# Optimization experiments

Hardware: AMD Instinct MI355X
Metric: run time of the kernel (lower is better)

Reference implementation:

```python
import jax, jax.numpy as jnp
import numpy as np

B, N, DIN, DINNER, DOUT, W = 4, 8192, 512, 512, 512, 128


def setup_inputs() -> dict:
    key = jax.random.key(0)
    k1, k2, k3 = jax.random.split(key, 3)
    x = jax.random.normal(k1, (B, N, DIN), jnp.float32)
    # torch Linear weights: (out_features, in_features)
    w_qkv = jax.random.normal(k2, (3 * DINNER, DIN), jnp.float32) * (DIN ** -0.5)
    w_out = jax.random.normal(k3, (DOUT, DINNER), jnp.float32) * (DINNER ** -0.5)
    b_out = jnp.zeros((DOUT,), jnp.float32)
    return {"x": x, "w_qkv": w_qkv, "w_out": w_out, "b_out": b_out}


def reference(x, w_qkv, w_out, b_out):
    b, n, _ = x.shape
    w = W
    scale = DINNER ** -0.5
    pad = (-n) % w  # pad_to_multiple along seq dim (static)
    xp = jnp.pad(x, ((0, 0), (0, pad), (0, 0)))
    qkv = jnp.einsum('bnd,ed->bne', xp, w_qkv)  # to_qkv, no bias
    q, k, v = jnp.split(qkv, 3, axis=-1)
    win = lambda t: t.reshape(b, -1, w, DINNER)  # b (w n) d -> b w n d
    q, k, v = win(q), win(k), win(v)
    # prepend one zero bucket to k, then overlap prev/current windows.
    kp = jnp.pad(k, ((0, 0), (1, 0), (0, 0), (0, 0)))
    k2 = jnp.concatenate((kp[:, :-1], kp[:, 1:]), axis=2)  # (b, nb, 2w, d)
    # NOTE: source bug replicated — v is also built from k, not v.
    v2 = jnp.concatenate((kp[:, :-1], kp[:, 1:]), axis=2)
    sim = jnp.einsum('bwid,bwjd->bwij', q, k2) * scale  # (b, nb, w, 2w)
    i, j = w, 2 * w
    mask = jnp.triu(jnp.ones((i, j), bool), j - i + 1)
    sim = jnp.where(mask, -jnp.finfo(sim.dtype).max, sim)
    attn = jax.nn.softmax(sim, axis=-1)
    out = jnp.einsum('bwij,bwjd->bwid', attn, v2)
    out = out.reshape(b, -1, DINNER)[:, :n]
    return jnp.einsum('bnd,od->bno', out, w_out) + b_out
```

## Files before the change

kernel.cpp:

```cpp
#include <hip/hip_runtime.h>
#include <cstdint>
#include <cstddef>

typedef float f32x4 __attribute__((ext_vector_type(4)));
typedef short s16x8 __attribute__((ext_vector_type(8)));
typedef short s16x4 __attribute__((ext_vector_type(4)));

#define MFMA_BF16(a, b, c) __builtin_amdgcn_mfma_f32_16x16x32_bf16((a), (b), (c), 0, 0, 0)

#define GLD16(g, l)                                                            \
  __builtin_amdgcn_global_load_lds(                                            \
      (const __attribute__((address_space(1))) void*)(g),                      \
      (__attribute__((address_space(3))) void*)(l), 16, 0, 0)

__device__ __forceinline__ unsigned short f2bf(float f) {
  unsigned int u = __float_as_uint(f);
  u += 0x7FFFu + ((u >> 16) & 1u);
  return (unsigned short)(u >> 16);
}

__device__ __forceinline__ s16x8 cvt8(const float* __restrict__ src) {
  const float4 f0 = *(const float4*)src;
  const float4 f1 = *(const float4*)(src + 4);
  s16x8 h;
  h[0] = (short)f2bf(f0.x); h[1] = (short)f2bf(f0.y);
  h[2] = (short)f2bf(f0.z); h[3] = (short)f2bf(f0.w);
  h[4] = (short)f2bf(f1.x); h[5] = (short)f2bf(f1.y);
  h[6] = (short)f2bf(f1.z); h[7] = (short)f2bf(f1.w);
  return h;
}

#define XN 16777216
#define WQN 524288
__global__ __launch_bounds__(256)
void cvt_bf16(const float* __restrict__ x, const float* __restrict__ wqkv,
              const float* __restrict__ wout, unsigned short* __restrict__ xb,
              unsigned short* __restrict__ wb, unsigned short* __restrict__ wob) {
  const size_t i = (size_t)(blockIdx.x * 256 + threadIdx.x) * 8;
  const float* src;
  unsigned short* dst;
  if (i < XN) { src = x + i; dst = xb + i; }
  else if (i < XN + WQN) { src = wqkv + (i - XN); dst = wb + (i - XN); }
  else { src = wout + (i - XN - WQN); dst = wob + (i - XN - WQN); }
  *(s16x8*)dst = cvt8(src);
}

__global__ __launch_bounds__(256)
void gemm_qk(const unsigned short* __restrict__ xb, const unsigned short* __restrict__ wb,
             unsigned short* __restrict__ Q, unsigned short* __restrict__ K) {
  __shared__ unsigned short As[128 * 64];
  __shared__ unsigned short Bs[128 * 64];
  const int t = threadIdx.x, lane = t & 63, wid = t >> 6;
  const int wm = wid >> 1, wn = wid & 1;
  const int nl = lane & 15, quad = lane >> 4;
  const int sub = lane >> 3, lblk = (lane & 7) ^ sub;
  const int l = blockIdx.x;
  const int xcd = l & 7, g = l >> 3;
  const int mt = (g >> 3) * 8 + xcd, nt = g & 7;
  const int m0 = mt * 128, n0 = nt * 128;

  const f32x4 zero = {0.f, 0.f, 0.f, 0.f};
  f32x4 acc[4][4];
#pragma unroll
  for (int i = 0; i < 4; ++i)
#pragma unroll
    for (int j = 0; j < 4; ++j) acc[i][j] = zero;

  const unsigned short* gX = xb + (size_t)(m0 + wid * 32 + sub) * 512 + lblk * 8;
  const unsigned short* gW = wb + (size_t)(n0 + wid * 32 + sub) * 512 + lblk * 8;

  for (int kc = 0; kc < 512; kc += 64) {
#pragma unroll
    for (int ii = 0; ii < 4; ++ii) {
      GLD16(gW + kc + (size_t)(ii * 8) * 512, &As[(wid * 32 + ii * 8) * 64]);
      GLD16(gX + kc + (size_t)(ii * 8) * 512, &Bs[(wid * 32 + ii * 8) * 64]);
    }
    __syncthreads();
#pragma unroll
    for (int ks = 0; ks < 2; ++ks) {
      s16x8 af[4], bf[4];
#pragma unroll
      for (int i = 0; i < 4; ++i)
        af[i] = *(const s16x8*)&As[(wm * 64 + i * 16 + nl) * 64 +
                                   (((ks * 4 + quad) ^ (nl & 7)) * 8)];
#pragma unroll
      for (int j = 0; j < 4; ++j)
        bf[j] = *(const s16x8*)&Bs[(wn * 64 + j * 16 + nl) * 64 +
                                   (((ks * 4 + quad) ^ (nl & 7)) * 8)];
#pragma unroll
      for (int i = 0; i < 4; ++i)
#pragma unroll
        for (int j = 0; j < 4; ++j) acc[i][j] = MFMA_BF16(af[i], bf[j], acc[i][j]);
    }
    __syncthreads();
  }
#pragma unroll
  for (int i = 0; i < 4; ++i) {
    const int n = n0 + wm * 64 + i * 16 + quad * 4;
    unsigned short* base = (n < 512 ? Q : K);
    const int nn = n & 511;
#pragma unroll
    for (int j = 0; j < 4; ++j) {
      const int m = m0 + wn * 64 + j * 16 + nl;
      s16x4 h;
#pragma unroll
      for (int r = 0; r < 4; ++r) h[r] = (short)f2bf(acc[i][j][r]);
      *(s16x4*)&base[(size_t)m * 512 + nn] = h;
    }
  }
}

__global__ __launch_bounds__(256)
void gemm_kwt(const unsigned short* __restrict__ K, const unsigned short* __restrict__ wob,
              unsigned short* __restrict__ KWT) {
  __shared__ unsigned short As[128 * 64];
  __shared__ unsigned short Bs[128 * 64];
  const int t = threadIdx.x, lane = t & 63, wid = t >> 6;
  const int wm = wid >> 1, wn = wid & 1;
  const int nl = lane & 15, quad = lane >> 4;
  const int sub = lane >> 3, lblk = (lane & 7) ^ sub;
  const int l = blockIdx.x;
  const int xcd = l & 7, g = l >> 3;
  const int mt = (g >> 2) * 8 + xcd, nt = g & 3;
  const int m0 = mt * 128, n0 = nt * 128;

  const f32x4 zero = {0.f, 0.f, 0.f, 0.f};
  f32x4 acc[4][4];
#pragma unroll
  for (int i = 0; i < 4; ++i)
#pragma unroll
    for (int j = 0; j < 4; ++j) acc[i][j] = zero;

  const unsigned short* gA = K + (size_t)(m0 + wid * 32 + sub) * 512 + lblk * 8;
  const unsigned short* gB = wob + (size_t)(n0 + wid * 32 + sub) * 512 + lblk * 8;

  for (int kc = 0; kc < 512; kc += 64) {
#pragma unroll
    for (int ii = 0; ii < 4; ++ii) {
      GLD16(gA + kc + (size_t)(ii * 8) * 512, &As[(wid * 32 + ii * 8) * 64]);
      GLD16(gB + kc + (size_t)(ii * 8) * 512, &Bs[(wid * 32 + ii * 8) * 64]);
    }
    __syncthreads();
#pragma unroll
    for (int ks = 0; ks < 2; ++ks) {
      s16x8 af[4], bf[4];
#pragma unroll
      for (int i = 0; i < 4; ++i)
        af[i] = *(const s16x8*)&As[(wm * 64 + i * 16 + nl) * 64 +
                                   (((ks * 4 + quad) ^ (nl & 7)) * 8)];
#pragma unroll
      for (int j = 0; j < 4; ++j)
        bf[j] = *(const s16x8*)&Bs[(wn * 64 + j * 16 + nl) * 64 +
                                   (((ks * 4 + quad) ^ (nl & 7)) * 8)];
#pragma unroll
      for (int i = 0; i < 4; ++i)
#pragma unroll
        for (int j = 0; j < 4; ++j) acc[i][j] = MFMA_BF16(af[i], bf[j], acc[i][j]);
    }
    __syncthreads();
  }
#pragma unroll
  for (int i = 0; i < 4; ++i) {
    const int ms = m0 + wm * 64 + i * 16 + quad * 4;
    const int b = ms >> 13, ns = ms & 8191;
#pragma unroll
    for (int j = 0; j < 4; ++j) {
      const int o = n0 + wn * 64 + j * 16 + nl;
      s16x4 h;
#pragma unroll
      for (int r = 0; r < 4; ++r) h[r] = (short)f2bf(acc[i][j][r]);
      *(s16x4*)&KWT[(size_t)(b * 512 + o) * 8192 + ns] = h;
    }
  }
}

__global__ __launch_bounds__(256)
void attn64(const unsigned short* __restrict__ Q, const unsigned short* __restrict__ K,
            const unsigned short* __restrict__ KWT, const float* __restrict__ bias,
            float* __restrict__ out) {
  __shared__ unsigned short Ps[64 * 256];
  __shared__ float redm[256];
  __shared__ float reds[256];
  const int t = threadIdx.x, lane = t & 63, wid = t >> 6;
  const int wn = wid;
  const int nl = lane & 15, quad = lane >> 4;
  const int bx = blockIdx.x;
  const int xcd = bx & 7, half = (bx >> 3) & 1, g = bx >> 4;
  const int wb = g * 8 + xcd, b = wb >> 6, w = wb & 63;

  const f32x4 zero = {0.f, 0.f, 0.f, 0.f};
  f32x4 acc[4][4];
#pragma unroll
  for (int i = 0; i < 4; ++i)
#pragma unroll
    for (int j = 0; j < 4; ++j) acc[i][j] = zero;

  const unsigned short* Qb = Q + (size_t)(b * 8192 + w * 128 + half * 64) * 512;
  const unsigned short* Kb = K + (size_t)(b * 8192) * 512;

  const unsigned short* qptr[4];
  const unsigned short* kptr[4];
#pragma unroll
  for (int i = 0; i < 4; ++i) qptr[i] = Qb + (size_t)(i * 16 + nl) * 512;
#pragma unroll
  for (int j = 0; j < 4; ++j) {
    int seq = w * 128 - 128 + wn * 64 + j * 16 + nl;
    if (seq < 0) seq = 0;
    kptr[j] = Kb + (size_t)seq * 512;
  }

#pragma unroll 2
  for (int kc = 0; kc < 512; kc += 64) {
#pragma unroll
    for (int ks = 0; ks < 2; ++ks) {
      const int off = kc + (ks * 4 + quad) * 8;
      s16x8 af[4], bf[4];
#pragma unroll
      for (int i = 0; i < 4; ++i) af[i] = *(const s16x8*)(qptr[i] + off);
#pragma unroll
      for (int j = 0; j < 4; ++j) bf[j] = *(const s16x8*)(kptr[j] + off);
      __builtin_amdgcn_s_setprio(1);
#pragma unroll
      for (int i = 0; i < 4; ++i)
#pragma unroll
        for (int j = 0; j < 4; ++j) acc[i][j] = MFMA_BF16(af[i], bf[j], acc[i][j]);
      __builtin_amdgcn_s_setprio(0);
    }
  }

  const float scale = 0.04419417382415922f;
  float rmax[4][4];
#pragma unroll
  for (int i = 0; i < 4; ++i) {
#pragma unroll
    for (int r = 0; r < 4; ++r) {
      const int qrow = half * 64 + i * 16 + quad * 4 + r;
      float mx = -3.4e38f;
#pragma unroll
      for (int j = 0; j < 4; ++j) {
        const int col = wn * 64 + j * 16 + nl;
        float v = acc[i][j][r] * scale;
        if (col >= 128 && col - 128 > qrow) v = -3.0e38f;
        if (w == 0 && col < 128) v = 0.0f;
        acc[i][j][r] = v;
        mx = fmaxf(mx, v);
      }
      rmax[i][r] = mx;
    }
  }
#pragma unroll
  for (int off = 1; off < 16; off <<= 1)
#pragma unroll
    for (int i = 0; i < 4; ++i)
#pragma unroll
      for (int r = 0; r < 4; ++r)
        rmax[i][r] = fmaxf(rmax[i][r], __shfl_xor(rmax[i][r], off, 64));
  if (nl == 0) {
#pragma unroll
    for (int i = 0; i < 4; ++i)
#pragma unroll
      for (int r = 0; r < 4; ++r)
        redm[(i * 16 + quad * 4 + r) * 4 + wn] = rmax[i][r];
  }
  __syncthreads();
  float rsum[4][4];
#pragma unroll
  for (int i = 0; i < 4; ++i) {
#pragma unroll
    for (int r = 0; r < 4; ++r) {
      const f32x4 mv = *(const f32x4*)&redm[(i * 16 + quad * 4 + r) * 4];
      const float m = fmaxf(fmaxf(mv[0], mv[1]), fmaxf(mv[2], mv[3]));
      float s = 0.f;
#pragma unroll
      for (int j = 0; j < 4; ++j) {
        const float p = __expf(acc[i][j][r] - m);
        acc[i][j][r] = p;
        s += p;
      }
      rsum[i][r] = s;
    }
  }
#pragma unroll
  for (int off = 1; off < 16; off <<= 1)
#pragma unroll
    for (int i = 0; i < 4; ++i)
#pragma unroll
      for (int r = 0; r < 4; ++r) rsum[i][r] += __shfl_xor(rsum[i][r], off, 64);
  if (nl == 0) {
#pragma unroll
    for (int i = 0; i < 4; ++i)
#pragma unroll
      for (int r = 0; r < 4; ++r)
        reds[(i * 16 + quad * 4 + r) * 4 + wn] = rsum[i][r];
  }
  __syncthreads();
#pragma unroll
  for (int i = 0; i < 4; ++i) {
#pragma unroll
    for (int r = 0; r < 4; ++r) {
      const int row = i * 16 + quad * 4 + r;
      const f32x4 sv = *(const f32x4*)&reds[row * 4];
      const float inv = 1.0f / (sv[0] + sv[1] + sv[2] + sv[3]);
#pragma unroll
      for (int j = 0; j < 4; ++j) {
        const int col = wn * 64 + j * 16 + nl;
        float pv = acc[i][j][r] * inv;
        if (w == 0 && col < 128) pv = 0.0f;
        const int cb = col >> 3;
        Ps[row * 256 + (((cb ^ (row & 7)) << 3) | (col & 7))] = f2bf(pv);
      }
    }
  }
  __syncthreads();

  const int seqbase = w * 128 - 128;
#pragma unroll 1
  for (int och = 0; och < 4; ++och) {
    f32x4 acc2[4][2];
#pragma unroll
    for (int i = 0; i < 4; ++i)
#pragma unroll
      for (int j = 0; j < 2; ++j) acc2[i][j] = zero;
    const unsigned short* bp0 =
        KWT + (size_t)(b * 512 + och * 128 + wn * 32 + nl) * 8192;
    const unsigned short* bp1 = bp0 + (size_t)16 * 8192;
#pragma unroll
    for (int kch = 0; kch < 4; ++kch) {
#pragma unroll
      for (int ks = 0; ks < 2; ++ks) {
        int sq = seqbase + kch * 64 + (ks * 4 + quad) * 8;
        if (sq < 0) sq = 0;
        const int kb = kch * 8 + ks * 4 + quad;
        s16x8 af[4], bf[2];
#pragma unroll
        for (int i = 0; i < 4; ++i)
          af[i] = *(const s16x8*)&Ps[(i * 16 + nl) * 256 + ((kb ^ (nl & 7)) << 3)];
        bf[0] = *(const s16x8*)(bp0 + sq);
        bf[1] = *(const s16x8*)(bp1 + sq);
        __builtin_amdgcn_s_setprio(1);
#pragma unroll
        for (int i = 0; i < 4; ++i) {
          acc2[i][0] = MFMA_BF16(af[i], bf[0], acc2[i][0]);
          acc2[i][1] = MFMA_BF16(af[i], bf[1], acc2[i][1]);
        }
        __builtin_amdgcn_s_setprio(0);
      }
    }
#pragma unroll
    for (int i = 0; i < 4; ++i) {
      const int seq = w * 128 + half * 64 + i * 16 + quad * 4;
      float* dst = out + (size_t)(b * 8192 + seq) * 512;
#pragma unroll
      for (int j = 0; j < 2; ++j) {
        const int o = och * 128 + wn * 32 + j * 16 + nl;
        const float bo = bias[o];
#pragma unroll
        for (int r = 0; r < 4; ++r) dst[(size_t)r * 512 + o] = acc2[i][j][r] + bo;
      }
    }
  }
}

extern "C" void kernel_launch(void* const* d_in, const int* in_sizes, int n_in,
                              void* d_out, int out_size, void* d_ws, size_t ws_size,
                              hipStream_t stream) {
  const float* x = (const float*)d_in[0];
  const float* w_qkv = (const float*)d_in[1];
  const float* w_out = (const float*)d_in[2];
  const float* b_out = (const float*)d_in[3];
  float* out = (float*)d_out;

  char* ws = (char*)d_ws;
  unsigned short* Q = (unsigned short*)ws;
  unsigned short* K = (unsigned short*)(ws + (size_t)33554432);
  unsigned short* xb = (unsigned short*)(ws + (size_t)67108864);
  unsigned short* KWT = (unsigned short*)(ws + (size_t)67108864);
  unsigned short* wb = (unsigned short*)(ws + (size_t)100663296);
  unsigned short* wob = (unsigned short*)(ws + (size_t)100663296 + 1048576);

  cvt_bf16<<<dim3(8576), dim3(256), 0, stream>>>(x, w_qkv, w_out, xb, wb, wob);
  gemm_qk<<<dim3(2048), dim3(256), 0, stream>>>(xb, wb, Q, K);
  gemm_kwt<<<dim3(1024), dim3(256), 0, stream>>>(K, wob, KWT);
  attn64<<<dim3(512), dim3(256), 0, stream>>>(Q, K, KWT, b_out, out);
}
```

Before: 255.3 us.

## Stage Q/K and KWT tiles through LDS with double-buffered async global_load_lds

Measured after the change: 245.2 us. 1.04x faster.

```diff
diff --git a/kernel.cpp b/kernel.cpp
--- a/kernel.cpp
+++ b/kernel.cpp
@@ -178,16 +178,59 @@
 void attn64(const unsigned short* __restrict__ Q, const unsigned short* __restrict__ K,
             const unsigned short* __restrict__ KWT, const float* __restrict__ bias,
             float* __restrict__ out) {
-  __shared__ unsigned short Ps[64 * 256];
-  __shared__ float redm[256];
-  __shared__ float reds[256];
+  __shared__ __align__(16) char smem[81920];
+  unsigned short* const Qb0 = (unsigned short*)smem;
+  unsigned short* const Qb1 = (unsigned short*)(smem + 8192);
+  unsigned short* const Kb0 = (unsigned short*)(smem + 16384);
+  unsigned short* const Kb1 = (unsigned short*)(smem + 49152);
+  float* const redm = (float*)(smem + 8192);
+  float* const reds = (float*)(smem + 9216);
+  unsigned short* const Ps = (unsigned short*)smem;
+  unsigned short* const B20 = (unsigned short*)(smem + 32768);
+  unsigned short* const B21 = (unsigned short*)(smem + 49152);
+
   const int t = threadIdx.x, lane = t & 63, wid = t >> 6;
   const int wn = wid;
   const int nl = lane & 15, quad = lane >> 4;
+  const int sub = lane >> 3, lblk = (lane & 7) ^ sub;
   const int bx = blockIdx.x;
   const int xcd = bx & 7, half = (bx >> 3) & 1, g = bx >> 4;
   const int wb = g * 8 + xcd, b = wb >> 6, w = wb & 63;
 
+  const unsigned short* Qg = Q + (size_t)(b * 8192 + w * 128 + half * 64) * 512;
+  const unsigned short* Kg = K + (size_t)(b * 8192) * 512;
+  const unsigned short* KWTb = KWT + (size_t)(b * 512) * 8192;
+  const int seqbase = w * 128 - 128;
+
+#define STAGE_P1(kcc, qb, kb)                                                  \
+  do {                                                                         \
+    _Pragma("unroll") for (int ii = 0; ii < 2; ++ii)                           \
+        GLD16(Qg + (size_t)(wid * 16 + ii * 8 + sub) * 512 + (kcc) + lblk * 8, \
+              (qb) + (wid * 16 + ii * 8) * 64);                                \
+    _Pragma("unroll") for (int ii = 0; ii < 8; ++ii) {                         \
+      int sq_ = seqbase + wid * 64 + ii * 8 + sub;                             \
+      if (sq_ < 0) sq_ = 0;                                                    \
+      GLD16(Kg + (size_t)sq_ * 512 + (kcc) + lblk * 8,                         \
+            (kb) + (wid * 64 + ii * 8) * 64);                                  \
+    }                                                                          \
+  } while (0)
+
+#define STAGE_B2(tt, bb)                                                       \
+  do {                                                                         \
+    const int och_ = (tt) >> 2, kch_ = (tt) & 3;                               \
+    int sq_ = seqbase + kch_ * 64 + lblk * 8;                                  \
+    if (sq_ < 0) sq_ = 0;                                                      \
+    _Pragma("unroll") for (int ii = 0; ii < 4; ++ii)                           \
+        GLD16(KWTb + (size_t)(och_ * 128 + wid * 32 + ii * 8 + sub) * 8192 + sq_, \
+              (bb) + (wid * 32 + ii * 8) * 64);                                \
+  } while (0)
+
+  float bo[4][2];
+#pragma unroll
+  for (int och = 0; och < 4; ++och)
+#pragma unroll
+    for (int j = 0; j < 2; ++j) bo[och][j] = bias[och * 128 + wn * 32 + j * 16 + nl];
+
   const f32x4 zero = {0.f, 0.f, 0.f, 0.f};
   f32x4 acc[4][4];
 #pragma unroll
@@ -195,30 +238,31 @@
 #pragma unroll
     for (int j = 0; j < 4; ++j) acc[i][j] = zero;
 
-  const unsigned short* Qb = Q + (size_t)(b * 8192 + w * 128 + half * 64) * 512;
-  const unsigned short* Kb = K + (size_t)(b * 8192) * 512;
-
-  const unsigned short* qptr[4];
-  const unsigned short* kptr[4];
-#pragma unroll
-  for (int i = 0; i < 4; ++i) qptr[i] = Qb + (size_t)(i * 16 + nl) * 512;
-#pragma unroll
-  for (int j = 0; j < 4; ++j) {
-    int seq = w * 128 - 128 + wn * 64 + j * 16 + nl;
-    if (seq < 0) seq = 0;
-    kptr[j] = Kb + (size_t)seq * 512;
-  }
-
-#pragma unroll 2
-  for (int kc = 0; kc < 512; kc += 64) {
+  STAGE_P1(0, Qb0, Kb0);
+#pragma unroll
+  for (int s = 0; s < 8; ++s) {
+    unsigned short* const qb = (s & 1) ? Qb1 : Qb0;
+    unsigned short* const kb = (s & 1) ? Kb1 : Kb0;
+    if (s < 7) {
+      STAGE_P1((s + 1) * 64, (s & 1) ? Qb0 : Qb1, (s & 1) ? Kb0 : Kb1);
+      asm volatile("s_waitcnt vmcnt(10)" ::: "memory");
+    } else {
+      STAGE_B2(0, B20);
+      asm volatile("s_waitcnt vmcnt(4)" ::: "memory");
+    }
+    __builtin_amdgcn_s_barrier();
+    asm volatile("" ::: "memory");
 #pragma unroll
     for (int ks = 0; ks < 2; ++ks) {
-      const int off = kc + (ks * 4 + quad) * 8;
       s16x8 af[4], bf[4];
 #pragma unroll
-      for (int i = 0; i < 4; ++i) af[i] = *(const s16x8*)(qptr[i] + off);
-#pragma unroll
-      for (int j = 0; j < 4; ++j) bf[j] = *(const s16x8*)(kptr[j] + off);
+      for (int i = 0; i < 4; ++i)
+        af[i] = *(const s16x8*)&qb[(i * 16 + nl) * 64 +
+                                   (((ks * 4 + quad) ^ (nl & 7)) * 8)];
+#pragma unroll
+      for (int j = 0; j < 4; ++j)
+        bf[j] = *(const s16x8*)&kb[(wn * 64 + j * 16 + nl) * 64 +
+                                   (((ks * 4 + quad) ^ (nl & 7)) * 8)];
       __builtin_amdgcn_s_setprio(1);
 #pragma unroll
       for (int i = 0; i < 4; ++i)
@@ -226,7 +270,10 @@
         for (int j = 0; j < 4; ++j) acc[i][j] = MFMA_BF16(af[i], bf[j], acc[i][j]);
       __builtin_amdgcn_s_setprio(0);
     }
-  }
+    asm volatile("" ::: "memory");
+    __builtin_amdgcn_s_barrier();
+  }
+  STAGE_B2(1, B21);
 
   const float scale = 0.04419417382415922f;
   float rmax[4][4];
@@ -262,7 +309,9 @@
       for (int r = 0; r < 4; ++r)
         redm[(i * 16 + quad * 4 + r) * 4 + wn] = rmax[i][r];
   }
-  __syncthreads();
+  asm volatile("s_waitcnt lgkmcnt(0)" ::: "memory");
+  __builtin_amdgcn_s_barrier();
+  asm volatile("" ::: "memory");
   float rsum[4][4];
 #pragma unroll
   for (int i = 0; i < 4; ++i) {
@@ -293,72 +342,92 @@
       for (int r = 0; r < 4; ++r)
         reds[(i * 16 + quad * 4 + r) * 4 + wn] = rsum[i][r];
   }
-  __syncthreads();
+  asm volatile("s_waitcnt lgkmcnt(0)" ::: "memory");
+  __builtin_amdgcn_s_barrier();
+  asm volatile("" ::: "memory");
+  float invv[4][4];
+#pragma unroll
+  for (int i = 0; i < 4; ++i)
+#pragma unroll
+    for (int r = 0; r < 4; ++r) {
+      const f32x4 sv = *(const f32x4*)&reds[(i * 16 + quad * 4 + r) * 4];
+      invv[i][r] = 1.0f / (sv[0] + sv[1] + sv[2] + sv[3]);
+    }
+  asm volatile("s_waitcnt lgkmcnt(0)" ::: "memory");
+  __builtin_amdgcn_s_barrier();
+  asm volatile("" ::: "memory");
 #pragma unroll
   for (int i = 0; i < 4; ++i) {
 #pragma unroll
     for (int r = 0; r < 4; ++r) {
       const int row = i * 16 + quad * 4 + r;
-      const f32x4 sv = *(const f32x4*)&reds[row * 4];
-      const float inv = 1.0f / (sv[0] + sv[1] + sv[2] + sv[3]);
 #pragma unroll
       for (int j = 0; j < 4; ++j) {
         const int col = wn * 64 + j * 16 + nl;
-        float pv = acc[i][j][r] * inv;
+        float pv = acc[i][j][r] * invv[i][r];
         if (w == 0 && col < 128) pv = 0.0f;
         const int cb = col >> 3;
         Ps[row * 256 + (((cb ^ (row & 7)) << 3) | (col & 7))] = f2bf(pv);
       }
     }
   }
-  __syncthreads();
-
-  const int seqbase = w * 128 - 128;
-#pragma unroll 1
-  for (int och = 0; och < 4; ++och) {
-    f32x4 acc2[4][2];
-#pragma unroll
-    for (int i = 0; i < 4; ++i)
-#pragma unroll
-      for (int j = 0; j < 2; ++j) acc2[i][j] = zero;
-    const unsigned short* bp0 =
-        KWT + (size_t)(b * 512 + och * 128 + wn * 32 + nl) * 8192;
-    const unsigned short* bp1 = bp0 + (size_t)16 * 8192;
-#pragma unroll
-    for (int kch = 0; kch < 4; ++kch) {
-#pragma unroll
-      for (int ks = 0; ks < 2; ++ks) {
-        int sq = seqbase + kch * 64 + (ks * 4 + quad) * 8;
-        if (sq < 0) sq = 0;
-        const int kb = kch * 8 + ks * 4 + quad;
-        s16x8 af[4], bf[2];
-#pragma unroll
-        for (int i = 0; i < 4; ++i)
-          af[i] = *(const s16x8*)&Ps[(i * 16 + nl) * 256 + ((kb ^ (nl & 7)) << 3)];
-        bf[0] = *(const s16x8*)(bp0 + sq);
-        bf[1] = *(const s16x8*)(bp1 + sq);
-        __builtin_amdgcn_s_setprio(1);
-#pragma unroll
-        for (int i = 0; i < 4; ++i) {
-          acc2[i][0] = MFMA_BF16(af[i], bf[0], acc2[i][0]);
-          acc2[i][1] = MFMA_BF16(af[i], bf[1], acc2[i][1]);
+  asm volatile("s_waitcnt lgkmcnt(0)" ::: "memory");
+  __builtin_amdgcn_s_barrier();
+  asm volatile("" ::: "memory");
+
+  f32x4 acc2[4][2];
+#pragma unroll
+  for (int t2 = 0; t2 < 16; ++t2) {
+    const int och = t2 >> 2, kch = t2 & 3;
+    unsigned short* const bb = (t2 & 1) ? B21 : B20;
+    if (kch == 0) {
+#pragma unroll
+      for (int i = 0; i < 4; ++i)
+#pragma unroll
+        for (int j = 0; j < 2; ++j) acc2[i][j] = zero;
+    }
+    if (t2 < 15) asm volatile("s_waitcnt vmcnt(4)" ::: "memory");
+    else         asm volatile("s_waitcnt vmcnt(0)" ::: "memory");
+    __builtin_amdgcn_s_barrier();
+    asm volatile("" ::: "memory");
+#pragma unroll
+    for (int ks = 0; ks < 2; ++ks) {
+      const int kb2 = kch * 8 + ks * 4 + quad;
+      s16x8 af[4], bf[2];
+#pragma unroll
+      for (int i = 0; i < 4; ++i)
+        af[i] = *(const s16x8*)&Ps[(i * 16 + nl) * 256 + ((kb2 ^ (nl & 7)) << 3)];
+#pragma unroll
+      for (int j = 0; j < 2; ++j)
+        bf[j] = *(const s16x8*)&bb[(wn * 32 + j * 16 + nl) * 64 +
+                                   (((ks * 4 + quad) ^ (nl & 7)) * 8)];
+      __builtin_amdgcn_s_setprio(1);
+#pragma unroll
+      for (int i = 0; i < 4; ++i) {
+        acc2[i][0] = MFMA_BF16(af[i], bf[0], acc2[i][0]);
+        acc2[i][1] = MFMA_BF16(af[i], bf[1], acc2[i][1]);
+      }
+      __builtin_amdgcn_s_setprio(0);
+    }
+    asm volatile("" ::: "memory");
+    __builtin_amdgcn_s_barrier();
+    if (kch == 3) {
+#pragma unroll
+      for (int i = 0; i < 4; ++i) {
+        const int seq = w * 128 + half * 64 + i * 16 + quad * 4;
+        float* dst = out + (size_t)(b * 8192 + seq) * 512;
+#pragma unroll
+        for (int j = 0; j < 2; ++j) {
+          const int o = och * 128 + wn * 32 + j * 16 + nl;
+#pragma unroll
+          for (int r = 0; r < 4; ++r) dst[(size_t)r * 512 + o] = acc2[i][j][r] + bo[och][j];
         }
-        __builtin_amdgcn_s_setprio(0);
       }
     }
-#pragma unroll
-    for (int i = 0; i < 4; ++i) {
-      const int seq = w * 128 + half * 64 + i * 16 + quad * 4;
-      float* dst = out + (size_t)(b * 8192 + seq) * 512;
-#pragma unroll
-      for (int j = 0; j < 2; ++j) {
-        const int o = och * 128 + wn * 32 + j * 16 + nl;
-        const float bo = bias[o];
-#pragma unroll
-        for (int r = 0; r < 4; ++r) dst[(size_t)r * 512 + o] = acc2[i][j][r] + bo;
-      }
-    }
-  }
+    if (t2 < 14) STAGE_B2(t2 + 2, bb);
+  }
+#undef STAGE_P1
+#undef STAGE_B2
 }
 
 extern "C" void kernel_launch(void* const* d_in, const int* in_sizes, int n_in,
```
